# Performance work log

Hardware: AMD Instinct MI355X
Metric: run time of the kernel (lower is better)

Reference implementation:

```python
import jax, jax.numpy as jnp
import numpy as np

B, T, I, H, O = 256, 512, 128, 1024, 64

def setup_inputs() -> dict:
    key = jax.random.key(0)
    ks = jax.random.split(key, 6)
    s = lambda n: 1.0 / np.sqrt(n)
    return {
        "X": jax.random.normal(ks[0], (B, T, I), dtype=jnp.float32),
        "h0": jnp.zeros((B, H), dtype=jnp.float32),
        "W": jax.random.normal(ks[1], (H, I), dtype=jnp.float32) * s(I),
        "U": jax.random.normal(ks[2], (H, H), dtype=jnp.float32) * s(H),
        "U_b": jax.random.normal(ks[3], (H,), dtype=jnp.float32) * s(H),
        "V": jax.random.normal(ks[4], (O, H), dtype=jnp.float32) * s(H),
        "V_b": jax.random.normal(ks[5], (O,), dtype=jnp.float32) * s(H),
    }

def reference(X, h0, W, U, U_b, V, V_b):
    # Precompute input projections for all timesteps: [B,T,H]
    Xw = jnp.einsum('bti,hi->bth', X, W)

    def step(h, xw_t):
        h_new = jnp.tanh(xw_t + h @ U.T + U_b)  # [B,H]
        return h_new, h_new

    # scan over time: move T to leading axis
    h_last, hs = jax.lax.scan(step, h0, jnp.swapaxes(Xw, 0, 1))
    # hs: [T,B,H] -> outputs Y: [B,T,O]
    Y = jnp.einsum('tbh,oh->bto', hs, V) + V_b
    return Y, h_last
```

## Files before the change

### kernel.cpp

```cpp
#include <hip/hip_runtime.h>
#include <hip/hip_bf16.h>
#include <cstdint>
#include <cstddef>

typedef __attribute__((ext_vector_type(4))) float f32x4;
typedef __attribute__((ext_vector_type(8))) __bf16 bf16x8;
typedef __attribute__((ext_vector_type(8))) unsigned short u16x8;
typedef __attribute__((ext_vector_type(4))) unsigned short u16x4;

#define B_ 256
#define T_ 512
#define I_ 128
#define H_ 1024
#define O_ 64
#define KTOT 1152
#define RSTR 2304

__device__ inline unsigned short f2bf(float f){
  unsigned u = __builtin_bit_cast(unsigned, f);
  u += 0x7fffu + ((u >> 16) & 1u);
  return (unsigned short)(u >> 16);
}

__device__ inline float fast_tanh(float x){
  float e = __builtin_amdgcn_exp2f(x * 2.885390081777927f);
  return 1.0f - 2.0f * __builtin_amdgcn_rcpf(e + 1.0f);
}

__global__ void cast_h0(const float* __restrict__ in, unsigned short* __restrict__ out){
  int i = (blockIdx.x * 256 + threadIdx.x) * 4;
  f32x4 v = *reinterpret_cast<const f32x4*>(in + i);
  u16x4 o;
  #pragma unroll
  for (int k = 0; k < 4; ++k) o[k] = f2bf(v[k]);
  *reinterpret_cast<u16x4*>(out + i) = o;
}

__global__ void cast_V(const float* __restrict__ in, unsigned short* __restrict__ out){
  int i = (blockIdx.x * 256 + threadIdx.x) * 4;
  f32x4 v = *reinterpret_cast<const f32x4*>(in + i);
  u16x4 o;
  #pragma unroll
  for (int k = 0; k < 4; ++k) o[k] = f2bf(v[k]);
  *reinterpret_cast<u16x4*>(out + i) = o;
}

__device__ inline void gload_lds16_llc(const unsigned short* src, void* dst){
  __builtin_amdgcn_global_load_lds(
      (const __attribute__((address_space(1))) unsigned int*)src,
      (__attribute__((address_space(3))) unsigned int*)dst, 16, 0, 17);
}

__global__ __launch_bounds__(256, 1) void rnn_fused(
    const float* __restrict__ X, const float* __restrict__ U, const float* __restrict__ W,
    const float* __restrict__ Ubias, const unsigned short* __restrict__ Vbf,
    const float* __restrict__ Vbias,
    unsigned short* __restrict__ hbuf,
    float* __restrict__ Y,
    float* __restrict__ hlast,
    unsigned* __restrict__ flags){
  extern __shared__ char smem[];
  char* sUb = smem;
  char* sAb = smem + 73728;
  char* sTb = smem + 147456;

  const int tid = threadIdx.x;
  const int wid = tid >> 6, lane = tid & 63;
  const int la = lane & 15, lg = lane >> 4;
  const int bg = blockIdx.x & 7, ns = blockIdx.x >> 3;
  const int b0 = bg * 32, j0 = ns * 32;

  for (int it = 0; it < 18; ++it){
    int c  = it * 256 + tid;
    int r  = c / 144, cc = c % 144;
    const float* src = (cc < 128) ? (U + (size_t)(j0 + r) * H_ + cc * 8)
                                  : (W + (size_t)(j0 + r) * I_ + (cc - 128) * 8);
    f32x4 f0 = *reinterpret_cast<const f32x4*>(src);
    f32x4 f1 = *reinterpret_cast<const f32x4*>(src + 4);
    u16x8 o;
    #pragma unroll
    for (int k = 0; k < 4; ++k){ o[k] = f2bf(f0[k]); o[k + 4] = f2bf(f1[k]); }
    int boff = r * RSTR + ((cc * 16) ^ ((r & 7) << 4));
    *reinterpret_cast<u16x8*>(sUb + boff) = o;
  }

  const int mw = wid & 1, nw = wid >> 1;
  const int rowA = (mw * 16 + la) * RSTR;
  const int rowB = (nw * 16 + la) * RSTR;
  const int sw   = (la & 7) << 4;
  const int cA   = (lg * 16) ^ sw;
  const int jme  = j0 + nw * 16 + la;
  const float ubv = Ubias[jme];

  __syncthreads();

  bf16x8 ufr[36];
  #pragma unroll
  for (int ks = 0; ks < 36; ++ks)
    ufr[ks] = *reinterpret_cast<const bf16x8*>(sUb + rowB + ((ks * 64) ^ cA));

  const int xr = tid >> 3, xsub = tid & 7;
  f32x4 xp0, xp1, xp2, xp3;
  {
    const float* xs = X + ((size_t)(b0 + xr) * T_ + 0) * I_ + xsub * 16;
    xp0 = *reinterpret_cast<const f32x4*>(xs);
    xp1 = *reinterpret_cast<const f32x4*>(xs + 4);
    xp2 = *reinterpret_cast<const f32x4*>(xs + 8);
    xp3 = *reinterpret_cast<const f32x4*>(xs + 12);
  }

  for (int t = 0; t <= T_; ++t){
    const int dns = (t - 1) & 31;
    const bool turnA = (t >= 1) && (dns == ns);
    const bool turnB = (t >= 1) && ((dns ^ 16) == ns);
    if (t == T_ && !(turnA || turnB)) break;

    const unsigned short* cur = hbuf + (size_t)(t & 1) * (B_ * H_);
    unsigned short*       nxt = hbuf + (size_t)((t + 1) & 1) * (B_ * H_);

    if (tid < 32){
      while (__hip_atomic_load(&flags[bg * 32 + tid], __ATOMIC_RELAXED,
                               __HIP_MEMORY_SCOPE_AGENT) < (unsigned)t)
        __builtin_amdgcn_s_sleep(1);
    }
    __syncthreads();

    #pragma unroll
    for (int it = 0; it < 16; ++it){
      int q    = it * 4 + wid;
      int row  = q >> 1, half = q & 1;
      int swr  = (row & 7) << 4;
      int cb   = half * 1024 + lane * 16;
      int se   = (b0 + row) * H_ + (((cb ^ swr)) >> 1);
      gload_lds16_llc(cur + se, sAb + row * RSTR + half * 1024);
    }
    if (t < T_){
      int swr = (xr & 7) << 4;
      u16x8 o01, o23;
      #pragma unroll
      for (int k = 0; k < 4; ++k){
        o01[k] = f2bf(xp0[k]); o01[k + 4] = f2bf(xp1[k]);
        o23[k] = f2bf(xp2[k]); o23[k + 4] = f2bf(xp3[k]);
      }
      int cb = xsub * 32;
      *reinterpret_cast<u16x8*>(sAb + xr * RSTR + 2048 + (cb ^ swr))        = o01;
      *reinterpret_cast<u16x8*>(sAb + xr * RSTR + 2048 + ((cb + 16) ^ swr)) = o23;
    }
    __syncthreads();

    if (t < T_ - 1){
      const float* xs = X + ((size_t)(b0 + xr) * T_ + (t + 1)) * I_ + xsub * 16;
      xp0 = *reinterpret_cast<const f32x4*>(xs);
      xp1 = *reinterpret_cast<const f32x4*>(xs + 4);
      xp2 = *reinterpret_cast<const f32x4*>(xs + 8);
      xp3 = *reinterpret_cast<const f32x4*>(xs + 12);
    }

    if (t < T_){
      f32x4 acc0 = {0, 0, 0, 0}, acc1 = {0, 0, 0, 0};
      #pragma unroll
      for (int ks = 0; ks < 36; ++ks){
        bf16x8 a = *reinterpret_cast<const bf16x8*>(sAb + rowA + ((ks * 64) ^ cA));
        if (ks & 1) acc1 = __builtin_amdgcn_mfma_f32_16x16x32_bf16(a, ufr[ks], acc1, 0, 0, 0);
        else        acc0 = __builtin_amdgcn_mfma_f32_16x16x32_bf16(a, ufr[ks], acc0, 0, 0, 0);
      }

      const int jl = nw * 16 + la;
      #pragma unroll
      for (int v = 0; v < 4; ++v){
        int b = mw * 16 + lg * 4 + v;
        float pre = acc0[v] + acc1[v] + ubv;
        float hv  = fast_tanh(pre);
        unsigned short hb = f2bf(hv);
        if (t == T_ - 1) hlast[(size_t)(b0 + b) * H_ + jme] = hv;
        *reinterpret_cast<unsigned short*>(sTb + b * 64 + ((jl * 2) ^ ((b & 3) << 4))) = hb;
      }
      __syncthreads();

      {
        int br = tid >> 3, j0l = (tid & 7) * 4;
        u16x4 hv4 = *reinterpret_cast<const u16x4*>(sTb + br * 64 + ((j0l * 2) ^ ((br & 3) << 4)));
        uint64_t hp = __builtin_bit_cast(uint64_t, hv4);
        __hip_atomic_store((uint64_t*)(nxt + (size_t)(b0 + br) * H_ + j0 + j0l), hp,
                           __ATOMIC_RELAXED, __HIP_MEMORY_SCOPE_AGENT);
      }
      __syncthreads();

      if (tid == 0)
        __hip_atomic_store(&flags[bg * 32 + ns], (unsigned)(t + 1),
                           __ATOMIC_RELAXED, __HIP_MEMORY_SCOPE_AGENT);
    }

    if (turnA || turnB){
      const int rb0 = turnA ? 0 : 16;
      const int orow = wid * 16 + la;
      const unsigned short* vp = Vbf + (size_t)orow * H_ + lg * 8;
      f32x4 y = {0, 0, 0, 0};
      #pragma unroll 8
      for (int kt = 0; kt < 32; ++kt){
        bf16x8 a = *reinterpret_cast<const bf16x8*>(sAb + (rb0 + la) * RSTR + ((kt * 64) ^ cA));
        bf16x8 f = *reinterpret_cast<const bf16x8*>(vp + kt * 32);
        y = __builtin_amdgcn_mfma_f32_16x16x32_bf16(a, f, y, 0, 0, 0);
      }
      const float vb = Vbias[orow];
      #pragma unroll
      for (int v = 0; v < 4; ++v){
        int b = rb0 + lg * 4 + v;
        Y[((size_t)(b0 + b) * T_ + (t - 1)) * O_ + orow] = y[v] + vb;
      }
      __syncthreads();
    }
  }
}

extern "C" void kernel_launch(void* const* d_in, const int* in_sizes, int n_in,
                              void* d_out, int out_size, void* d_ws, size_t ws_size,
                              hipStream_t stream){
  const float* X  = (const float*)d_in[0];
  const float* h0 = (const float*)d_in[1];
  const float* W  = (const float*)d_in[2];
  const float* U  = (const float*)d_in[3];
  const float* Ub = (const float*)d_in[4];
  const float* V  = (const float*)d_in[5];
  const float* Vb = (const float*)d_in[6];
  float* Y     = (float*)d_out;
  float* hlast = Y + (size_t)B_ * T_ * O_;

  char* ws = (char*)d_ws;
  unsigned short* hbuf  = (unsigned short*)(ws);
  unsigned short* Vbf   = (unsigned short*)(ws + 1048576);
  unsigned*       flags = (unsigned*)(ws + 1179648);

  cast_h0<<<256, 256, 0, stream>>>(h0, hbuf);
  cast_V<<<64, 256, 0, stream>>>(V, Vbf);
  (void)hipMemsetAsync(flags, 0, 1024, stream);

  (void)hipFuncSetAttribute((const void*)rnn_fused,
                            hipFuncAttributeMaxDynamicSharedMemorySize, 149504);
  void* args[] = { (void*)&X, (void*)&U, (void*)&W, (void*)&Ub, (void*)&Vbf, (void*)&Vb,
                   (void*)&hbuf, (void*)&Y, (void*)&hlast, (void*)&flags };
  (void)hipLaunchCooperativeKernel((const void*)rnn_fused, dim3(256), dim3(256),
                                   args, 149504, stream);
}
```

Before: 2.346 ms.

## Cut per-step barriers with shuffle transpose and per-wave flag polling

The LDS staging of the new hidden tile, and its two barriers, are replaced by a register transpose built from lane shuffles before the packed 64-bit stores. Flag polling moves from one 32-thread group followed by a block barrier to per-wave polling of only the 16 producer flags whose columns that wave loads. The X tile write is hoisted ahead of the wait. The U staging buffer now aliases the activation buffer, which lowers the dynamic LDS request. The goal is to shorten the serial per-timestep critical path. The cost is extra shuffle work and more waves spinning on flags.

```diff
diff --git a/kernel.cpp b/kernel.cpp
--- a/kernel.cpp
+++ b/kernel.cpp
@@ -60,9 +60,7 @@
     float* __restrict__ hlast,
     unsigned* __restrict__ flags){
   extern __shared__ char smem[];
-  char* sUb = smem;
-  char* sAb = smem + 73728;
-  char* sTb = smem + 147456;
+  char* sAb = smem;
 
   const int tid = threadIdx.x;
   const int wid = tid >> 6, lane = tid & 63;
@@ -81,14 +79,13 @@
     #pragma unroll
     for (int k = 0; k < 4; ++k){ o[k] = f2bf(f0[k]); o[k + 4] = f2bf(f1[k]); }
     int boff = r * RSTR + ((cc * 16) ^ ((r & 7) << 4));
-    *reinterpret_cast<u16x8*>(sUb + boff) = o;
+    *reinterpret_cast<u16x8*>(smem + boff) = o;
   }
 
   const int mw = wid & 1, nw = wid >> 1;
   const int rowA = (mw * 16 + la) * RSTR;
   const int rowB = (nw * 16 + la) * RSTR;
-  const int sw   = (la & 7) << 4;
-  const int cA   = (lg * 16) ^ sw;
+  const int cA   = (lg * 16) ^ ((la & 7) << 4);
   const int jme  = j0 + nw * 16 + la;
   const float ubv = Ubias[jme];
 
@@ -97,7 +94,8 @@
   bf16x8 ufr[36];
   #pragma unroll
   for (int ks = 0; ks < 36; ++ks)
-    ufr[ks] = *reinterpret_cast<const bf16x8*>(sUb + rowB + ((ks * 64) ^ cA));
+    ufr[ks] = *reinterpret_cast<const bf16x8*>(smem + rowB + ((ks * 64) ^ cA));
+  __syncthreads();
 
   const int xr = tid >> 3, xsub = tid & 7;
   f32x4 xp0, xp1, xp2, xp3;
@@ -109,6 +107,8 @@
     xp3 = *reinterpret_cast<const f32x4*>(xs + 12);
   }
 
+  const int fbase = bg * 32 + (wid & 1) * 16;
+
   for (int t = 0; t <= T_; ++t){
     const int dns = (t - 1) & 31;
     const bool turnA = (t >= 1) && (dns == ns);
@@ -118,22 +118,6 @@
     const unsigned short* cur = hbuf + (size_t)(t & 1) * (B_ * H_);
     unsigned short*       nxt = hbuf + (size_t)((t + 1) & 1) * (B_ * H_);
 
-    if (tid < 32){
-      while (__hip_atomic_load(&flags[bg * 32 + tid], __ATOMIC_RELAXED,
-                               __HIP_MEMORY_SCOPE_AGENT) < (unsigned)t)
-        __builtin_amdgcn_s_sleep(1);
-    }
-    __syncthreads();
-
-    #pragma unroll
-    for (int it = 0; it < 16; ++it){
-      int q    = it * 4 + wid;
-      int row  = q >> 1, half = q & 1;
-      int swr  = (row & 7) << 4;
-      int cb   = half * 1024 + lane * 16;
-      int se   = (b0 + row) * H_ + (((cb ^ swr)) >> 1);
-      gload_lds16_llc(cur + se, sAb + row * RSTR + half * 1024);
-    }
     if (t < T_){
       int swr = (xr & 7) << 4;
       u16x8 o01, o23;
@@ -146,6 +130,21 @@
       *reinterpret_cast<u16x8*>(sAb + xr * RSTR + 2048 + (cb ^ swr))        = o01;
       *reinterpret_cast<u16x8*>(sAb + xr * RSTR + 2048 + ((cb + 16) ^ swr)) = o23;
     }
+
+    if (lane < 16){
+      while (__hip_atomic_load(&flags[fbase + lane], __ATOMIC_RELAXED,
+                               __HIP_MEMORY_SCOPE_AGENT) < (unsigned)t)
+        __builtin_amdgcn_s_sleep(1);
+    }
+
+    #pragma unroll
+    for (int it = 0; it < 16; ++it){
+      int q    = it * 4 + wid;
+      int row  = q >> 1, half = q & 1;
+      int cb   = half * 1024 + lane * 16;
+      int se   = (b0 + row) * H_ + ((cb ^ ((row & 7) << 4)) >> 1);
+      gload_lds16_llc(cur + se, sAb + row * RSTR + half * 1024);
+    }
     __syncthreads();
 
     if (t < T_ - 1){
@@ -165,31 +164,38 @@
         else        acc0 = __builtin_amdgcn_mfma_f32_16x16x32_bf16(a, ufr[ks], acc0, 0, 0, 0);
       }
 
-      const int jl = nw * 16 + la;
-      #pragma unroll
-      for (int v = 0; v < 4; ++v){
-        int b = mw * 16 + lg * 4 + v;
-        float pre = acc0[v] + acc1[v] + ubv;
-        float hv  = fast_tanh(pre);
-        unsigned short hb = f2bf(hv);
-        if (t == T_ - 1) hlast[(size_t)(b0 + b) * H_ + jme] = hv;
-        *reinterpret_cast<unsigned short*>(sTb + b * 64 + ((jl * 2) ^ ((b & 3) << 4))) = hb;
-      }
-      __syncthreads();
-
+      unsigned r0, r1, r2, r3;
       {
-        int br = tid >> 3, j0l = (tid & 7) * 4;
-        u16x4 hv4 = *reinterpret_cast<const u16x4*>(sTb + br * 64 + ((j0l * 2) ^ ((br & 3) << 4)));
-        uint64_t hp = __builtin_bit_cast(uint64_t, hv4);
-        __hip_atomic_store((uint64_t*)(nxt + (size_t)(b0 + br) * H_ + j0 + j0l), hp,
-                           __ATOMIC_RELAXED, __HIP_MEMORY_SCOPE_AGENT);
-      }
-      __syncthreads();
-
-      if (tid == 0)
-        __hip_atomic_store(&flags[bg * 32 + ns], (unsigned)(t + 1),
-                           __ATOMIC_RELAXED, __HIP_MEMORY_SCOPE_AGENT);
-    }
+        float hv[4];
+        #pragma unroll
+        for (int v = 0; v < 4; ++v){
+          int b = mw * 16 + lg * 4 + v;
+          hv[v] = fast_tanh(acc0[v] + acc1[v] + ubv);
+          if (t == T_ - 1) hlast[(size_t)(b0 + b) * H_ + jme] = hv[v];
+        }
+        r0 = f2bf(hv[0]); r1 = f2bf(hv[1]); r2 = f2bf(hv[2]); r3 = f2bf(hv[3]);
+      }
+      unsigned s;
+      s = __shfl_xor((lane & 1) ? r0 : r1, 1);
+      if (lane & 1) r0 = s; else r1 = s;
+      s = __shfl_xor((lane & 1) ? r2 : r3, 1);
+      if (lane & 1) r2 = s; else r3 = s;
+      s = __shfl_xor((lane & 2) ? r0 : r2, 2);
+      if (lane & 2) r0 = s; else r2 = s;
+      s = __shfl_xor((lane & 2) ? r1 : r3, 2);
+      if (lane & 2) r1 = s; else r3 = s;
+      uint64_t hp = (uint64_t)(r0 & 0xffffu) | ((uint64_t)(r1 & 0xffffu) << 16)
+                  | ((uint64_t)(r2 & 0xffffu) << 32) | ((uint64_t)(r3 & 0xffffu) << 48);
+      const int br = mw * 16 + lg * 4 + (la & 3);
+      const int jc = nw * 16 + (la & ~3);
+      __hip_atomic_store((uint64_t*)(nxt + (size_t)(b0 + br) * H_ + j0 + jc), hp,
+                         __ATOMIC_RELAXED, __HIP_MEMORY_SCOPE_AGENT);
+    }
+    __syncthreads();
+
+    if (t < T_ && tid == 0)
+      __hip_atomic_store(&flags[bg * 32 + ns], (unsigned)(t + 1),
+                         __ATOMIC_RELAXED, __HIP_MEMORY_SCOPE_AGENT);
 
     if (turnA || turnB){
       const int rb0 = turnA ? 0 : 16;
@@ -236,9 +242,9 @@
   (void)hipMemsetAsync(flags, 0, 1024, stream);
 
   (void)hipFuncSetAttribute((const void*)rnn_fused,
-                            hipFuncAttributeMaxDynamicSharedMemorySize, 149504);
+                            hipFuncAttributeMaxDynamicSharedMemorySize, 73728);
   void* args[] = { (void*)&X, (void*)&U, (void*)&W, (void*)&Ub, (void*)&Vbf, (void*)&Vb,
                    (void*)&hbuf, (void*)&Y, (void*)&hlast, (void*)&flags };
   (void)hipLaunchCooperativeKernel((const void*)rnn_fused, dim3(256), dim3(256),
-                                   args, 149504, stream);
-}
+                                   args, 73728, stream);
+}
```

New measurement: 2.477 ms. 5.6% more time.

## Tile hidden-state buffer into 32x32 blocks and overlap per-tile flag waits with loads

Applied to the files above, without the earlier changes.

The global hidden-state buffer is stored as contiguous swizzled 32x32 tiles, one per producer block, so each consumer loads a whole tile with linear 16-byte global-to-LDS copies. The single barrier-gated wait on all 32 flags becomes a per-wave wait per tile, so loads of ready tiles can start before slower producers finish. The U staging area in LDS is reused for the A buffer, cutting dynamic shared memory roughly in half. A fallback normal launch is added if the cooperative launch fails. The new tile layout and swizzles must match across the cast kernel, the store, the MFMA reads and the V projection.

```diff
diff --git a/kernel.cpp b/kernel.cpp
--- a/kernel.cpp
+++ b/kernel.cpp
@@ -13,8 +13,9 @@
 #define I_ 128
 #define H_ 1024
 #define O_ 64
-#define KTOT 1152
 #define RSTR 2304
+#define XOFF 65536
+#define TOFF 73728
 
 __device__ inline unsigned short f2bf(float f){
   unsigned u = __builtin_bit_cast(unsigned, f);
@@ -29,11 +30,14 @@
 
 __global__ void cast_h0(const float* __restrict__ in, unsigned short* __restrict__ out){
   int i = (blockIdx.x * 256 + threadIdx.x) * 4;
+  int b = i >> 10, j = i & 1023;
   f32x4 v = *reinterpret_cast<const f32x4*>(in + i);
   u16x4 o;
   #pragma unroll
   for (int k = 0; k < 4; ++k) o[k] = f2bf(v[k]);
-  *reinterpret_cast<u16x4*>(out + i) = o;
+  int r = b & 31, jc = j & 31, c = jc >> 3, w = jc & 7;
+  size_t oi = ((size_t)(b >> 5) * 32 + (j >> 5)) * 1024 + r * 32 + ((c ^ (r & 3)) * 8) + w;
+  *reinterpret_cast<u16x4*>(out + oi) = o;
 }
 
 __global__ void cast_V(const float* __restrict__ in, unsigned short* __restrict__ out){
@@ -60,9 +64,8 @@
     float* __restrict__ hlast,
     unsigned* __restrict__ flags){
   extern __shared__ char smem[];
-  char* sUb = smem;
-  char* sAb = smem + 73728;
-  char* sTb = smem + 147456;
+  char* sAb = smem;
+  char* sTb = smem + TOFF;
 
   const int tid = threadIdx.x;
   const int wid = tid >> 6, lane = tid & 63;
@@ -81,14 +84,13 @@
     #pragma unroll
     for (int k = 0; k < 4; ++k){ o[k] = f2bf(f0[k]); o[k + 4] = f2bf(f1[k]); }
     int boff = r * RSTR + ((cc * 16) ^ ((r & 7) << 4));
-    *reinterpret_cast<u16x8*>(sUb + boff) = o;
+    *reinterpret_cast<u16x8*>(smem + boff) = o;
   }
 
   const int mw = wid & 1, nw = wid >> 1;
-  const int rowA = (mw * 16 + la) * RSTR;
+  const int rowl = mw * 16 + la;
   const int rowB = (nw * 16 + la) * RSTR;
-  const int sw   = (la & 7) << 4;
-  const int cA   = (lg * 16) ^ sw;
+  const int cA   = (lg * 16) ^ ((la & 7) << 4);
   const int jme  = j0 + nw * 16 + la;
   const float ubv = Ubias[jme];
 
@@ -97,7 +99,8 @@
   bf16x8 ufr[36];
   #pragma unroll
   for (int ks = 0; ks < 36; ++ks)
-    ufr[ks] = *reinterpret_cast<const bf16x8*>(sUb + rowB + ((ks * 64) ^ cA));
+    ufr[ks] = *reinterpret_cast<const bf16x8*>(smem + rowB + ((ks * 64) ^ cA));
+  __syncthreads();
 
   const int xr = tid >> 3, xsub = tid & 7;
   f32x4 xp0, xp1, xp2, xp3;
@@ -109,6 +112,8 @@
     xp3 = *reinterpret_cast<const f32x4*>(xs + 12);
   }
 
+  const int aswz = (lg ^ (la & 3)) << 4;
+
   for (int t = 0; t <= T_; ++t){
     const int dns = (t - 1) & 31;
     const bool turnA = (t >= 1) && (dns == ns);
@@ -118,33 +123,30 @@
     const unsigned short* cur = hbuf + (size_t)(t & 1) * (B_ * H_);
     unsigned short*       nxt = hbuf + (size_t)((t + 1) & 1) * (B_ * H_);
 
-    if (tid < 32){
-      while (__hip_atomic_load(&flags[bg * 32 + tid], __ATOMIC_RELAXED,
-                               __HIP_MEMORY_SCOPE_AGENT) < (unsigned)t)
-        __builtin_amdgcn_s_sleep(1);
-    }
-    __syncthreads();
-
-    #pragma unroll
-    for (int it = 0; it < 16; ++it){
-      int q    = it * 4 + wid;
-      int row  = q >> 1, half = q & 1;
-      int swr  = (row & 7) << 4;
-      int cb   = half * 1024 + lane * 16;
-      int se   = (b0 + row) * H_ + (((cb ^ swr)) >> 1);
-      gload_lds16_llc(cur + se, sAb + row * RSTR + half * 1024);
-    }
     if (t < T_){
-      int swr = (xr & 7) << 4;
       u16x8 o01, o23;
       #pragma unroll
       for (int k = 0; k < 4; ++k){
         o01[k] = f2bf(xp0[k]); o01[k + 4] = f2bf(xp1[k]);
         o23[k] = f2bf(xp2[k]); o23[k + 4] = f2bf(xp3[k]);
       }
-      int cb = xsub * 32;
-      *reinterpret_cast<u16x8*>(sAb + xr * RSTR + 2048 + (cb ^ swr))        = o01;
-      *reinterpret_cast<u16x8*>(sAb + xr * RSTR + 2048 + ((cb + 16) ^ swr)) = o23;
+      int sw = (xr & 7) << 1;
+      char* xb = sAb + XOFF + xr * 256;
+      int c0 = xsub * 2;
+      *reinterpret_cast<u16x8*>(xb + ((c0 ^ sw) << 4))       = o01;
+      *reinterpret_cast<u16x8*>(xb + (((c0 + 1) ^ sw) << 4)) = o23;
+    }
+
+    #pragma unroll 1
+    for (int i = 0; i < 8; ++i){
+      int p = wid * 8 + i;
+      const unsigned* fp = &flags[bg * 32 + p];
+      while (!__all(__hip_atomic_load(fp, __ATOMIC_RELAXED,
+                                      __HIP_MEMORY_SCOPE_AGENT) >= (unsigned)t))
+        __builtin_amdgcn_s_sleep(1);
+      const unsigned short* src = cur + ((size_t)(bg * 32 + p) << 10) + lane * 8;
+      gload_lds16_llc(src,       sAb + p * 2048);
+      gload_lds16_llc(src + 512, sAb + p * 2048 + 1024);
     }
     __syncthreads();
 
@@ -159,18 +161,25 @@
     if (t < T_){
       f32x4 acc0 = {0, 0, 0, 0}, acc1 = {0, 0, 0, 0};
       #pragma unroll
-      for (int ks = 0; ks < 36; ++ks){
-        bf16x8 a = *reinterpret_cast<const bf16x8*>(sAb + rowA + ((ks * 64) ^ cA));
+      for (int ks = 0; ks < 32; ++ks){
+        bf16x8 a = *reinterpret_cast<const bf16x8*>(sAb + ks * 2048 + rowl * 64 + aswz);
         if (ks & 1) acc1 = __builtin_amdgcn_mfma_f32_16x16x32_bf16(a, ufr[ks], acc1, 0, 0, 0);
         else        acc0 = __builtin_amdgcn_mfma_f32_16x16x32_bf16(a, ufr[ks], acc0, 0, 0, 0);
       }
+      #pragma unroll
+      for (int ks = 32; ks < 36; ++ks){
+        int cr = (ks - 32) * 4 + lg;
+        bf16x8 a = *reinterpret_cast<const bf16x8*>(
+            sAb + XOFF + rowl * 256 + ((cr ^ ((rowl & 7) << 1)) << 4));
+        if (ks & 1) acc1 = __builtin_amdgcn_mfma_f32_16x16x32_bf16(a, ufr[ks], acc1, 0, 0, 0);
+        else        acc0 = __builtin_amdgcn_mfma_f32_16x16x32_bf16(a, ufr[ks], acc0, 0, 0, 0);
+      }
 
       const int jl = nw * 16 + la;
       #pragma unroll
       for (int v = 0; v < 4; ++v){
         int b = mw * 16 + lg * 4 + v;
-        float pre = acc0[v] + acc1[v] + ubv;
-        float hv  = fast_tanh(pre);
+        float hv = fast_tanh(acc0[v] + acc1[v] + ubv);
         unsigned short hb = f2bf(hv);
         if (t == T_ - 1) hlast[(size_t)(b0 + b) * H_ + jme] = hv;
         *reinterpret_cast<unsigned short*>(sTb + b * 64 + ((jl * 2) ^ ((b & 3) << 4))) = hb;
@@ -178,10 +187,9 @@
       __syncthreads();
 
       {
-        int br = tid >> 3, j0l = (tid & 7) * 4;
-        u16x4 hv4 = *reinterpret_cast<const u16x4*>(sTb + br * 64 + ((j0l * 2) ^ ((br & 3) << 4)));
+        u16x4 hv4 = *reinterpret_cast<const u16x4*>(sTb + tid * 8);
         uint64_t hp = __builtin_bit_cast(uint64_t, hv4);
-        __hip_atomic_store((uint64_t*)(nxt + (size_t)(b0 + br) * H_ + j0 + j0l), hp,
+        __hip_atomic_store((uint64_t*)(nxt + ((size_t)(bg * 32 + ns) << 10) + tid * 4), hp,
                            __ATOMIC_RELAXED, __HIP_MEMORY_SCOPE_AGENT);
       }
       __syncthreads();
@@ -198,7 +206,8 @@
       f32x4 y = {0, 0, 0, 0};
       #pragma unroll 8
       for (int kt = 0; kt < 32; ++kt){
-        bf16x8 a = *reinterpret_cast<const bf16x8*>(sAb + (rb0 + la) * RSTR + ((kt * 64) ^ cA));
+        bf16x8 a = *reinterpret_cast<const bf16x8*>(
+            sAb + kt * 2048 + (rb0 + la) * 64 + aswz);
         bf16x8 f = *reinterpret_cast<const bf16x8*>(vp + kt * 32);
         y = __builtin_amdgcn_mfma_f32_16x16x32_bf16(a, f, y, 0, 0, 0);
       }
@@ -236,9 +245,13 @@
   (void)hipMemsetAsync(flags, 0, 1024, stream);
 
   (void)hipFuncSetAttribute((const void*)rnn_fused,
-                            hipFuncAttributeMaxDynamicSharedMemorySize, 149504);
+                            hipFuncAttributeMaxDynamicSharedMemorySize, 75776);
   void* args[] = { (void*)&X, (void*)&U, (void*)&W, (void*)&Ub, (void*)&Vbf, (void*)&Vb,
                    (void*)&hbuf, (void*)&Y, (void*)&hlast, (void*)&flags };
-  (void)hipLaunchCooperativeKernel((const void*)rnn_fused, dim3(256), dim3(256),
-                                   args, 149504, stream);
-}
+  hipError_t rc = hipLaunchCooperativeKernel((const void*)rnn_fused, dim3(256), dim3(256),
+                                             args, 75776, stream);
+  if (rc != hipSuccess){
+    rnn_fused<<<dim3(256), dim3(256), 75776, stream>>>(X, U, W, Ub, Vbf, Vb,
+                                                       hbuf, Y, hlast, flags);
+  }
+}
```

Result: slower. 3.022 ms (+28.8%).
